# Kernel optimization log

Measured on AMD Instinct MI355X. Metric: run time of the kernel, lower is better.

The kernel has to match this reference:

```python
import jax, jax.numpy as jnp
import numpy as np

T, B, N, D, O = 128, 8, 512, 256, 1


def _xavier(key, shape):
    # matches nn.init.xavier_normal_ (gain=1): std = sqrt(2/(fan_in+fan_out))
    std = np.sqrt(2.0 / (shape[0] + shape[1])).astype(np.float32)
    return jax.random.normal(key, shape, jnp.float32) * std


def setup_inputs() -> dict:
    key = jax.random.key(0)
    ks = jax.random.split(key, 7)
    return {
        "x": jax.random.normal(ks[0], (T, B, D), jnp.float32),
        "w_mult": _xavier(ks[1], (N, D)),
        "b_mult": _xavier(ks[2], (N, 1))[:, 0],   # stored (N,1) in torch; used as bias vector
        "w_add": _xavier(ks[3], (N, N)),
        "b_add": _xavier(ks[4], (N, 1))[:, 0],
        "w_final": _xavier(ks[5], (O, N)),
        "b_final": _xavier(ks[6], (O, 1))[:, 0],
        "lmbda_mult": jnp.float32(1.0),
        "lmbda_add": jnp.float32(1.0),
        "eta_mult": jnp.float32(-0.5),
        "eta_add": jnp.float32(-0.5),
        "Store": 0,
        "Batch": 0,
    }


def reference(x, w_mult, b_mult, w_add, b_add, w_final, b_final,
              lmbda_mult, lmbda_add, eta_mult, eta_add, Store, Batch):
    # Store=False / Batch=False branch of HebbFF, vmapped over B sequences
    # and scanned over T timesteps. Fast-weight state: A_mult [B,N,D], A_add [B,N,N].
    Bt = x.shape[1]
    Nh, Dd = w_mult.shape
    lam_m = jax.nn.sigmoid(lmbda_mult)
    lam_a = jax.nn.sigmoid(lmbda_add)

    def step(carry, x_t):
        A_m, A_a = carry                      # [B,N,D], [B,N,N]
        # h_mult = tanh((w_mult * A_mult) @ x + w_mult @ x + b_mult)
        h_m = jnp.tanh(jnp.einsum('bnd,bd->bn', w_mult * A_m, x_t)
                       + x_t @ w_mult.T + b_mult)          # [B,N]
        A_m = lam_m * A_m + eta_mult * jnp.einsum('bn,bd->bnd', h_m, x_t)
        # h_add = sigmoid((w_add + A_add) @ h_mult + b_add)
        h_a = jax.nn.sigmoid(jnp.einsum('bnm,bm->bn', A_a, h_m)
                             + h_m @ w_add.T + b_add)      # [B,N]
        A_a = lam_a * A_a + eta_add * jnp.einsum('bn,bm->bnm', h_a, h_m)
        y_t = jax.nn.sigmoid(h_a @ w_final.T + b_final)    # [B,O]
        return (A_m, A_a), y_t

    A_m0 = jnp.zeros((Bt, Nh, Dd), x.dtype)
    A_a0 = jnp.zeros((Bt, Nh, Nh), x.dtype)
    _, ys = jax.lax.scan(step, (A_m0, A_a0), x)            # ys: [T,B,O]
    return ys
```

## Files before the change

kernel.cpp:

```cpp
#include <hip/hip_runtime.h>
#include <cstdint>


#define T_ 128
#define B_ 8
#define N_ 512
#define D_ 256
#define NTHREADS 512
#define CH 16
#define NC (T_ / CH)
#define HOFF (T_ * B_ * N_)

typedef float v2f __attribute__((ext_vector_type(2)));

__device__ __forceinline__ v2f v2(float s) { v2f r; r.x = s; r.y = s; return r; }

__device__ __forceinline__ void load_lds16(const float* g, float* l) {
  __builtin_amdgcn_global_load_lds(
      (const __attribute__((address_space(1))) uint32_t*)(const void*)g,
      (__attribute__((address_space(3))) uint32_t*)(void*)l, 16, 0, 0);
}

__device__ __forceinline__ float dpp_wave_sum(float v) {
#define UPD(ctrl)                                                              \
  v += __int_as_float(                                                         \
      __builtin_amdgcn_update_dpp(0, __float_as_int(v), ctrl, 0xf, 0xf, true))
  UPD(0x111); UPD(0x112); UPD(0x114); UPD(0x118); UPD(0x142); UPD(0x143);
#undef UPD
  return __int_as_float(__builtin_amdgcn_readlane(__float_as_int(v), 63));
}
__device__ __forceinline__ float sigmoid_f(float z) {
  return __builtin_amdgcn_rcpf(1.f + __expf(-z));
}
__device__ __forceinline__ float tanh_f(float z) {
  return 1.f - 2.f * __builtin_amdgcn_rcpf(1.f + __expf(2.f * z));
}

__global__ void __launch_bounds__(NTHREADS, 2)
hebb_part1(const float* __restrict__ x, const float* __restrict__ w_mult,
           const float* __restrict__ b_mult, const float* __restrict__ p_lm,
           const float* __restrict__ p_em, float* __restrict__ ws) {
  const int g = blockIdx.x & 7, sub = blockIdx.x >> 3;
  const int wave = threadIdx.x >> 6, lane = threadIdx.x & 63;
  const int n0 = (sub * 8 + wave) * 2;

  __shared__ float xs[2][CH][D_];

  const float lam = sigmoid_f(p_lm[0]);
  const float eta = p_em[0];
  const v2f lam2 = v2(lam), klam2 = v2(1.f - lam);

  v2f wm[2][2], Bm[2][2];
  float bm[2];
#pragma unroll
  for (int r = 0; r < 2; ++r) {
    bm[r] = b_mult[n0 + r];
#pragma unroll
    for (int c = 0; c < 2; ++c) {
      wm[r][c] = *(const v2f*)&w_mult[(n0 + r) * D_ + c * 128 + 2 * lane];
      Bm[r][c] = v2(1.f);
    }
  }

  auto issue_stage = [&](int c) {
#pragma unroll
    for (int k = 0; k < 2; ++k) {
      const int row = k * 8 + wave;
      const int trow = c * CH + row;
      load_lds16(&x[(trow * B_ + g) * D_ + 4 * lane], &xs[c & 1][row][0]);
    }
  };

  issue_stage(0);
  __syncthreads();

  v2f xv[2][2];
  auto ldx = [&](int buf, int cb, int tl) {
    xv[buf][0] = *(const v2f*)&xs[cb][tl][2 * lane];
    xv[buf][1] = *(const v2f*)&xs[cb][tl][128 + 2 * lane];
  };

  for (int c = 0; c < NC; ++c) {
    if (c + 1 < NC) issue_stage(c + 1);
    const int cb = c & 1;
    ldx(0, cb, 0);
#pragma unroll
    for (int tl = 0; tl < CH; ++tl) {
      const int buf = tl & 1;
      if (tl + 1 < CH) ldx(buf ^ 1, cb, tl + 1);
      float hmv[2];
#pragma unroll
      for (int r = 0; r < 2; ++r) {
        v2f a = wm[r][0] * xv[buf][0] * Bm[r][0];
        a = __builtin_elementwise_fma(wm[r][1] * xv[buf][1], Bm[r][1], a);
        const float z = dpp_wave_sum(a.x + a.y) + bm[r];
        const float hm = tanh_f(z);
        hmv[r] = hm;
        const v2f c2 = v2(eta * hm);
#pragma unroll
        for (int cc = 0; cc < 2; ++cc) {
          v2f inner = __builtin_elementwise_fma(c2, xv[buf][cc], klam2);
          Bm[r][cc] = __builtin_elementwise_fma(lam2, Bm[r][cc], inner);
        }
      }
      if (lane == 0) {
        v2f hv2; hv2.x = hmv[0]; hv2.y = hmv[1];
        *(v2f*)(ws + ((c * CH + tl) * B_ + g) * N_ + n0) = hv2;
      }
    }
    __syncthreads();
  }
}

__global__ void __launch_bounds__(NTHREADS, 2)
hebb_part2(const float* __restrict__ w_add, const float* __restrict__ b_add,
           const float* __restrict__ w_final, const float* __restrict__ p_la,
           const float* __restrict__ p_ea, float* __restrict__ ws) {
  const int g = blockIdx.x & 7, sub = blockIdx.x >> 3;
  const int wave = threadIdx.x >> 6, lane = threadIdx.x & 63;
  const int n0 = (sub * 8 + wave) * 2;

  __shared__ float hs[2][CH][N_];

  const float lam = sigmoid_f(p_la[0]);
  const float eta = p_ea[0];
  const v2f lam2 = v2(lam);
  const float klam = 1.f - lam;

  v2f Sa[2][4], wb[2][4];
  float ba[2], wf[2];
#pragma unroll
  for (int r = 0; r < 2; ++r) {
    ba[r] = b_add[n0 + r];
    wf[r] = w_final[n0 + r];
#pragma unroll
    for (int c = 0; c < 4; ++c) {
      const v2f wa = *(const v2f*)&w_add[(n0 + r) * N_ + c * 128 + 2 * lane];
      Sa[r][c] = wa;
      wb[r][c] = wa * klam;
    }
  }

  const float* hsrc = ws;
  float* part = ws + HOFF;

  auto issue_stage = [&](int c) {
#pragma unroll
    for (int k = 0; k < 2; ++k) {
      const int row = k * 8 + wave;
      const int trow = c * CH + row;
#pragma unroll
      for (int j = 0; j < 2; ++j)
        load_lds16(&hsrc[(trow * B_ + g) * N_ + j * 256 + 4 * lane],
                   &hs[c & 1][row][j * 256]);
    }
  };

  issue_stage(0);
  __syncthreads();

  v2f hv[2][4];
  auto ldh = [&](int buf, int cb, int tl) {
#pragma unroll
    for (int cc = 0; cc < 4; ++cc)
      hv[buf][cc] = *(const v2f*)&hs[cb][tl][cc * 128 + 2 * lane];
  };

  for (int c = 0; c < NC; ++c) {
    if (c + 1 < NC) issue_stage(c + 1);
    const int cb = c & 1;
    ldh(0, cb, 0);
#pragma unroll
    for (int tl = 0; tl < CH; ++tl) {
      const int buf = tl & 1;
      if (tl + 1 < CH) ldh(buf ^ 1, cb, tl + 1);
      float py = 0.f;
#pragma unroll
      for (int r = 0; r < 2; ++r) {
        v2f a0 = Sa[r][0] * hv[buf][0];
        v2f a1 = Sa[r][1] * hv[buf][1];
        a0 = __builtin_elementwise_fma(Sa[r][2], hv[buf][2], a0);
        a1 = __builtin_elementwise_fma(Sa[r][3], hv[buf][3], a1);
        const v2f a = a0 + a1;
        const float z = dpp_wave_sum(a.x + a.y) + ba[r];
        const float ha = sigmoid_f(z);
        const v2f c2 = v2(eta * ha);
#pragma unroll
        for (int cc = 0; cc < 4; ++cc) {
          v2f inner = __builtin_elementwise_fma(c2, hv[buf][cc], wb[r][cc]);
          Sa[r][cc] = __builtin_elementwise_fma(lam2, Sa[r][cc], inner);
        }
        py = __builtin_fmaf(wf[r], ha, py);
      }
      if (lane == 0)
        part[((c * CH + tl) * B_ + g) * 256 + sub * 8 + wave] = py;
    }
    __syncthreads();
  }
}

__global__ void __launch_bounds__(NTHREADS)
hebb_final(const float* __restrict__ ws, const float* __restrict__ b_final,
           float* __restrict__ out) {
  const int wave = threadIdx.x >> 6, lane = threadIdx.x & 63;
  const int tb = blockIdx.x * 8 + wave;
  const float4 v = *(const float4*)(ws + HOFF + tb * 256 + lane * 4);
  const float s = dpp_wave_sum((v.x + v.y) + (v.z + v.w));
  if (lane == 0) out[tb] = sigmoid_f(s + b_final[0]);
}

extern "C" void kernel_launch(void* const* d_in, const int* in_sizes, int n_in,
                              void* d_out, int out_size, void* d_ws,
                              size_t ws_size, hipStream_t stream) {
  const float* x       = (const float*)d_in[0];
  const float* w_mult  = (const float*)d_in[1];
  const float* b_mult  = (const float*)d_in[2];
  const float* w_add   = (const float*)d_in[3];
  const float* b_add   = (const float*)d_in[4];
  const float* w_final = (const float*)d_in[5];
  const float* b_final = (const float*)d_in[6];
  const float* p_lm    = (const float*)d_in[7];
  const float* p_la    = (const float*)d_in[8];
  const float* p_em    = (const float*)d_in[9];
  const float* p_ea    = (const float*)d_in[10];
  float* out = (float*)d_out;
  float* ws  = (float*)d_ws;

  hipLaunchKernelGGL(hebb_part1, dim3(256), dim3(NTHREADS), 0, stream,
                     x, w_mult, b_mult, p_lm, p_em, ws);
  hipLaunchKernelGGL(hebb_part2, dim3(256), dim3(NTHREADS), 0, stream,
                     w_add, b_add, w_final, p_la, p_ea, ws);
  hipLaunchKernelGGL(hebb_final, dim3(128), dim3(NTHREADS), 0, stream,
                     ws, b_final, out);
}
```

Baseline: 76.65 us.

## Replace additive fast-weight recurrence with unrolled kernel-matrix formulation and blocked scan

The additive Hebbian recurrence is rewritten algebraically. The A_add state contribution becomes a sum over past steps, weighted by lambda powers times the h_mult Gram products. A mid kernel computes w_add·h_mult for all timesteps plus the decayed Gram matrix, then a small scan kernel resolves the sigmoid recurrence in 16-step blocks, and a final kernel applies w_final. This removes the per-step N×N state update but adds an extra launch, O(T²) Gram work and a serial scan with limited parallelism (64 blocks). The old path is kept as a fallback when the workspace is too small.

```diff
diff --git a/kernel.cpp b/kernel.cpp
--- a/kernel.cpp
+++ b/kernel.cpp
@@ -9,11 +9,18 @@
 #define NTHREADS 512
 #define CH 16
 #define NC (T_ / CH)
+
+#define HP_OFF 0
+#define Z0_OFF 524288
+#define WS_OFF 1048576
+#define WS_NEED ((size_t)(1048576 + 131072) * 4)
+
 #define HOFF (T_ * B_ * N_)
 
 typedef float v2f __attribute__((ext_vector_type(2)));
 
 __device__ __forceinline__ v2f v2(float s) { v2f r; r.x = s; r.y = s; return r; }
+__device__ __forceinline__ v2f mk2(float a, float b) { v2f r; r.x = a; r.y = b; return r; }
 
 __device__ __forceinline__ void load_lds16(const float* g, float* l) {
   __builtin_amdgcn_global_load_lds(
@@ -36,14 +43,14 @@
   return 1.f - 2.f * __builtin_amdgcn_rcpf(1.f + __expf(2.f * z));
 }
 
+
 __global__ void __launch_bounds__(NTHREADS, 2)
-hebb_part1(const float* __restrict__ x, const float* __restrict__ w_mult,
-           const float* __restrict__ b_mult, const float* __restrict__ p_lm,
-           const float* __restrict__ p_em, float* __restrict__ ws) {
+np_part1(const float* __restrict__ x, const float* __restrict__ w_mult,
+         const float* __restrict__ b_mult, const float* __restrict__ p_lm,
+         const float* __restrict__ p_em, float* __restrict__ ws) {
   const int g = blockIdx.x & 7, sub = blockIdx.x >> 3;
   const int wave = threadIdx.x >> 6, lane = threadIdx.x & 63;
   const int n0 = (sub * 8 + wave) * 2;
-
   __shared__ float xs[2][CH][D_];
 
   const float lam = sigmoid_f(p_lm[0]);
@@ -66,20 +73,21 @@
 #pragma unroll
     for (int k = 0; k < 2; ++k) {
       const int row = k * 8 + wave;
-      const int trow = c * CH + row;
-      load_lds16(&x[(trow * B_ + g) * D_ + 4 * lane], &xs[c & 1][row][0]);
-    }
-  };
-
+      load_lds16(&x[((c * CH + row) * B_ + g) * D_ + 4 * lane],
+                 &xs[c & 1][row][0]);
+    }
+  };
   issue_stage(0);
   __syncthreads();
 
+  float* hp = ws + HP_OFF;
   v2f xv[2][2];
   auto ldx = [&](int buf, int cb, int tl) {
     xv[buf][0] = *(const v2f*)&xs[cb][tl][2 * lane];
     xv[buf][1] = *(const v2f*)&xs[cb][tl][128 + 2 * lane];
   };
 
+  float ph0 = 0.f, ph1 = 0.f;
   for (int c = 0; c < NC; ++c) {
     if (c + 1 < NC) issue_stage(c + 1);
     const int cb = c & 1;
@@ -103,8 +111,252 @@
           Bm[r][cc] = __builtin_elementwise_fma(lam2, Bm[r][cc], inner);
         }
       }
+      if (tl & 1) {
+        if (lane == 0) {
+          const int t2 = (c * CH + tl) >> 1;
+          *(float4*)(hp + ((t2 * B_ + g) * N_ + n0) * 2) =
+              make_float4(ph0, hmv[0], ph1, hmv[1]);
+        }
+      } else {
+        ph0 = hmv[0];
+        ph1 = hmv[1];
+      }
+    }
+    __syncthreads();
+  }
+}
+
+__global__ void __launch_bounds__(NTHREADS, 2)
+np_mid(const float* __restrict__ w_add, const float* __restrict__ b_add,
+       const float* __restrict__ p_la, const float* __restrict__ p_ea,
+       float* __restrict__ ws) {
+  __shared__ float hl[8192];
+  const int tid = threadIdx.x;
+  const int wave = tid >> 6, lane = tid & 63;
+  const float* hp = ws + HP_OFF;
+  float* z0 = ws + Z0_OFF;
+  float* Wsc = ws + WS_OFF;
+  const float lam = sigmoid_f(p_la[0]);
+  const float eta = p_ea[0];
+
+  if (blockIdx.x < 128) {
+    const int tbc = blockIdx.x;
+    const float* src = hp + tbc * 4 * 1024;
+#pragma unroll
+    for (int i = 0; i < 2; ++i)
+      load_lds16(src + (wave * 2 + i) * 256 + lane * 4,
+                 hl + (wave * 2 + i) * 256);
+    __syncthreads();
+    const int n = tid;
+    v2f acc[4] = {v2(0.f), v2(0.f), v2(0.f), v2(0.f)};
+    const float* wrow = w_add + n * N_;
+    for (int m = 0; m < N_; m += 4) {
+      const float4 w4 = *(const float4*)&wrow[m];
+#pragma unroll
+      for (int p = 0; p < 4; ++p) {
+        const float4 ha = *(const float4*)&hl[p * 1024 + m * 2];
+        const float4 hb = *(const float4*)&hl[p * 1024 + m * 2 + 4];
+        acc[p] = __builtin_elementwise_fma(v2(w4.x), mk2(ha.x, ha.y), acc[p]);
+        acc[p] = __builtin_elementwise_fma(v2(w4.y), mk2(ha.z, ha.w), acc[p]);
+        acc[p] = __builtin_elementwise_fma(v2(w4.z), mk2(hb.x, hb.y), acc[p]);
+        acc[p] = __builtin_elementwise_fma(v2(w4.w), mk2(hb.z, hb.w), acc[p]);
+      }
+    }
+    const float bad = b_add[n];
+#pragma unroll
+    for (int p = 0; p < 4; ++p) {
+      const int tbp = tbc * 4 + p;
+      const int tbe = tbp + 8 * (tbp >> 3);
+      z0[tbe * N_ + n] = acc[p].x + bad;
+      z0[(tbe + 8) * N_ + n] = acc[p].y + bad;
+    }
+  } else {
+    const int gb = blockIdx.x - 128;
+    const int b = gb >> 3, tc = gb & 7;
+    {
+      const int q = wave;
+      const float* rsrc = hp + ((tc * 8 + q) * 8 + b) * 1024;
+#pragma unroll
+      for (int sgm = 0; sgm < 4; ++sgm)
+        load_lds16(rsrc + sgm * 256 + lane * 4, hl + q * 1024 + sgm * 256);
+    }
+    __syncthreads();
+    const int s = tid & 127, tq = tid >> 7;
+    const int tmax = tc * 16 + tq * 4 + 3;
+    v2f acc[2] = {v2(0.f), v2(0.f)};
+    if (s < tmax) {
+      const float* srow = hp + ((s >> 1) * 8 + b) * 1024 + (s & 1);
+#pragma unroll 4
+      for (int n = 0; n < N_; ++n) {
+        const float hs = srow[n * 2];
+        const float2 hA = *(const float2*)&hl[(tq * 2 + 0) * 1024 + n * 2];
+        const float2 hB = *(const float2*)&hl[(tq * 2 + 1) * 1024 + n * 2];
+        acc[0] = __builtin_elementwise_fma(v2(hs), mk2(hA.x, hA.y), acc[0]);
+        acc[1] = __builtin_elementwise_fma(v2(hs), mk2(hB.x, hB.y), acc[1]);
+      }
+    }
+    const float l2lam = __log2f(lam);
+#pragma unroll
+    for (int i = 0; i < 4; ++i) {
+      const int t = tc * 16 + tq * 4 + i;
+      const float gv = (i & 1) ? acc[i >> 1].y : acc[i >> 1].x;
+      float w = 0.f;
+      if (s < t) w = eta * exp2f((float)(t - 1 - s) * l2lam) * gv;
+      Wsc[(b * T_ + t) * T_ + s] = w;
+    }
+  }
+}
+
+__global__ void __launch_bounds__(NTHREADS, 1)
+np_scan(float* __restrict__ ws) {
+  __shared__ float ul[T_][64];
+  __shared__ float zx[16][64];
+  __shared__ float Wtile[16][16];
+  const int b = blockIdx.x >> 3, nc = blockIdx.x & 7;
+  const int wave = threadIdx.x >> 6, lane = threadIdx.x & 63;
+  float* z0 = ws + Z0_OFF;
+  const float* Wb = ws + WS_OFF + b * T_ * T_;
+
+  const int ta = 2 * wave, tb2 = 2 * wave + 1;
+  const int ncol = nc * 64 + lane;
+
+  float za = z0[(ta * B_ + b) * N_ + ncol];
+  float zb = z0[(tb2 * B_ + b) * N_ + ncol];
+
+  for (int j = 0; j < 8; ++j) {
+    const int t0 = j * 16;
+    const float* wga = Wb + (t0 + ta) * T_;
+    const float* wgb = Wb + (t0 + tb2) * T_;
+    float zna = 0.f, znb = 0.f;
+    if (j < 7) {
+      zna = z0[((t0 + 16 + ta) * B_ + b) * N_ + ncol];
+      znb = z0[((t0 + 16 + tb2) * B_ + b) * N_ + ncol];
+    }
+    if (lane < 4) {
+      *(float4*)&Wtile[ta][lane * 4] = *(const float4*)&wga[t0 + lane * 4];
+      *(float4*)&Wtile[tb2][lane * 4] = *(const float4*)&wgb[t0 + lane * 4];
+    }
+    float ha0 = 0.f, ha1 = 0.f, hb0 = 0.f, hb1 = 0.f;
+#pragma unroll 2
+    for (int s4 = 0; s4 < t0; s4 += 4) {
+      const float4 wa = *(const float4*)&wga[s4];
+      const float4 wb = *(const float4*)&wgb[s4];
+      const float u0 = ul[s4 + 0][lane], u1 = ul[s4 + 1][lane];
+      const float u2 = ul[s4 + 2][lane], u3 = ul[s4 + 3][lane];
+      ha0 = __builtin_fmaf(wa.x, u0, ha0);
+      ha1 = __builtin_fmaf(wa.y, u1, ha1);
+      ha0 = __builtin_fmaf(wa.z, u2, ha0);
+      ha1 = __builtin_fmaf(wa.w, u3, ha1);
+      hb0 = __builtin_fmaf(wb.x, u0, hb0);
+      hb1 = __builtin_fmaf(wb.y, u1, hb1);
+      hb0 = __builtin_fmaf(wb.z, u2, hb0);
+      hb1 = __builtin_fmaf(wb.w, u3, hb1);
+    }
+    zx[ta][lane] = za + (ha0 + ha1);
+    zx[tb2][lane] = zb + (hb0 + hb1);
+    __syncthreads();
+    if (wave == 0) {
+      float z[16], uv[16];
+#pragma unroll
+      for (int i = 0; i < 16; ++i) z[i] = zx[i][lane];
+#pragma unroll
+      for (int i = 0; i < 16; ++i) {
+        const float u = sigmoid_f(z[i]);
+        uv[i] = u;
+        z0[((t0 + i) * B_ + b) * N_ + ncol] = u;
+#pragma unroll
+        for (int tt = i + 1; tt < 16; ++tt)
+          z[tt] = __builtin_fmaf(u, Wtile[tt][i], z[tt]);
+      }
+#pragma unroll
+      for (int i = 0; i < 16; ++i) ul[t0 + i][lane] = uv[i];
+    }
+    __syncthreads();
+    za = zna;
+    zb = znb;
+  }
+}
+
+__global__ void __launch_bounds__(NTHREADS)
+np_final(const float* __restrict__ ws, const float* __restrict__ w_final,
+         const float* __restrict__ b_final, float* __restrict__ out) {
+  const int wave = threadIdx.x >> 6, lane = threadIdx.x & 63;
+  const int tb = blockIdx.x * 8 + wave;
+  const float* u = ws + Z0_OFF + tb * N_ + lane * 8;
+  const float4 a = *(const float4*)u, c = *(const float4*)(u + 4);
+  const float4 wa = *(const float4*)&w_final[lane * 8];
+  const float4 wc = *(const float4*)&w_final[lane * 8 + 4];
+  float d = a.x * wa.x + a.y * wa.y + a.z * wa.z + a.w * wa.w +
+            c.x * wc.x + c.y * wc.y + c.z * wc.z + c.w * wc.w;
+  d = dpp_wave_sum(d);
+  if (lane == 0) out[tb] = sigmoid_f(d + b_final[0]);
+}
+
+
+__global__ void __launch_bounds__(NTHREADS, 2)
+fb_part1(const float* __restrict__ x, const float* __restrict__ w_mult,
+         const float* __restrict__ b_mult, const float* __restrict__ p_lm,
+         const float* __restrict__ p_em, float* __restrict__ ws) {
+  const int g = blockIdx.x & 7, sub = blockIdx.x >> 3;
+  const int wave = threadIdx.x >> 6, lane = threadIdx.x & 63;
+  const int n0 = (sub * 8 + wave) * 2;
+  __shared__ float xs[2][CH][D_];
+  const float lam = sigmoid_f(p_lm[0]);
+  const float eta = p_em[0];
+  const v2f lam2 = v2(lam), klam2 = v2(1.f - lam);
+  v2f wm[2][2], Bm[2][2];
+  float bm[2];
+#pragma unroll
+  for (int r = 0; r < 2; ++r) {
+    bm[r] = b_mult[n0 + r];
+#pragma unroll
+    for (int c = 0; c < 2; ++c) {
+      wm[r][c] = *(const v2f*)&w_mult[(n0 + r) * D_ + c * 128 + 2 * lane];
+      Bm[r][c] = v2(1.f);
+    }
+  }
+  auto issue_stage = [&](int c) {
+#pragma unroll
+    for (int k = 0; k < 2; ++k) {
+      const int row = k * 8 + wave;
+      load_lds16(&x[((c * CH + row) * B_ + g) * D_ + 4 * lane],
+                 &xs[c & 1][row][0]);
+    }
+  };
+  issue_stage(0);
+  __syncthreads();
+  v2f xv[2][2];
+  auto ldx = [&](int buf, int cb, int tl) {
+    xv[buf][0] = *(const v2f*)&xs[cb][tl][2 * lane];
+    xv[buf][1] = *(const v2f*)&xs[cb][tl][128 + 2 * lane];
+  };
+  for (int c = 0; c < NC; ++c) {
+    if (c + 1 < NC) issue_stage(c + 1);
+    const int cb = c & 1;
+    ldx(0, cb, 0);
+#pragma unroll
+    for (int tl = 0; tl < CH; ++tl) {
+      const int buf = tl & 1;
+      if (tl + 1 < CH) ldx(buf ^ 1, cb, tl + 1);
+      float hmv[2];
+#pragma unroll
+      for (int r = 0; r < 2; ++r) {
+        v2f a = wm[r][0] * xv[buf][0] * Bm[r][0];
+        a = __builtin_elementwise_fma(wm[r][1] * xv[buf][1], Bm[r][1], a);
+        const float z = dpp_wave_sum(a.x + a.y) + bm[r];
+        const float hm = tanh_f(z);
+        hmv[r] = hm;
+        const v2f c2 = v2(eta * hm);
+#pragma unroll
+        for (int cc = 0; cc < 2; ++cc) {
+          v2f inner = __builtin_elementwise_fma(c2, xv[buf][cc], klam2);
+          Bm[r][cc] = __builtin_elementwise_fma(lam2, Bm[r][cc], inner);
+        }
+      }
       if (lane == 0) {
-        v2f hv2; hv2.x = hmv[0]; hv2.y = hmv[1];
+        v2f hv2;
+        hv2.x = hmv[0];
+        hv2.y = hmv[1];
         *(v2f*)(ws + ((c * CH + tl) * B_ + g) * N_ + n0) = hv2;
       }
     }
@@ -113,20 +365,17 @@
 }
 
 __global__ void __launch_bounds__(NTHREADS, 2)
-hebb_part2(const float* __restrict__ w_add, const float* __restrict__ b_add,
-           const float* __restrict__ w_final, const float* __restrict__ p_la,
-           const float* __restrict__ p_ea, float* __restrict__ ws) {
+fb_part2(const float* __restrict__ w_add, const float* __restrict__ b_add,
+         const float* __restrict__ w_final, const float* __restrict__ p_la,
+         const float* __restrict__ p_ea, float* __restrict__ ws) {
   const int g = blockIdx.x & 7, sub = blockIdx.x >> 3;
   const int wave = threadIdx.x >> 6, lane = threadIdx.x & 63;
   const int n0 = (sub * 8 + wave) * 2;
-
   __shared__ float hs[2][CH][N_];
-
   const float lam = sigmoid_f(p_la[0]);
   const float eta = p_ea[0];
   const v2f lam2 = v2(lam);
   const float klam = 1.f - lam;
-
   v2f Sa[2][4], wb[2][4];
   float ba[2], wf[2];
 #pragma unroll
@@ -140,32 +389,26 @@
       wb[r][c] = wa * klam;
     }
   }
-
   const float* hsrc = ws;
   float* part = ws + HOFF;
-
   auto issue_stage = [&](int c) {
 #pragma unroll
     for (int k = 0; k < 2; ++k) {
       const int row = k * 8 + wave;
-      const int trow = c * CH + row;
-#pragma unroll
-      for (int j = 0; j < 2; ++j)
-        load_lds16(&hsrc[(trow * B_ + g) * N_ + j * 256 + 4 * lane],
-                   &hs[c & 1][row][j * 256]);
-    }
-  };
-
+#pragma unroll
+      for (int jj = 0; jj < 2; ++jj)
+        load_lds16(&hsrc[((c * CH + row) * B_ + g) * N_ + jj * 256 + 4 * lane],
+                   &hs[c & 1][row][jj * 256]);
+    }
+  };
   issue_stage(0);
   __syncthreads();
-
   v2f hv[2][4];
   auto ldh = [&](int buf, int cb, int tl) {
 #pragma unroll
     for (int cc = 0; cc < 4; ++cc)
       hv[buf][cc] = *(const v2f*)&hs[cb][tl][cc * 128 + 2 * lane];
   };
-
   for (int c = 0; c < NC; ++c) {
     if (c + 1 < NC) issue_stage(c + 1);
     const int cb = c & 1;
@@ -200,14 +443,15 @@
 }
 
 __global__ void __launch_bounds__(NTHREADS)
-hebb_final(const float* __restrict__ ws, const float* __restrict__ b_final,
-           float* __restrict__ out) {
+fb_final(const float* __restrict__ ws, const float* __restrict__ b_final,
+         float* __restrict__ out) {
   const int wave = threadIdx.x >> 6, lane = threadIdx.x & 63;
   const int tb = blockIdx.x * 8 + wave;
   const float4 v = *(const float4*)(ws + HOFF + tb * 256 + lane * 4);
   const float s = dpp_wave_sum((v.x + v.y) + (v.z + v.w));
   if (lane == 0) out[tb] = sigmoid_f(s + b_final[0]);
 }
+
 
 extern "C" void kernel_launch(void* const* d_in, const int* in_sizes, int n_in,
                               void* d_out, int out_size, void* d_ws,
@@ -226,10 +470,20 @@
   float* out = (float*)d_out;
   float* ws  = (float*)d_ws;
 
-  hipLaunchKernelGGL(hebb_part1, dim3(256), dim3(NTHREADS), 0, stream,
-                     x, w_mult, b_mult, p_lm, p_em, ws);
-  hipLaunchKernelGGL(hebb_part2, dim3(256), dim3(NTHREADS), 0, stream,
-                     w_add, b_add, w_final, p_la, p_ea, ws);
-  hipLaunchKernelGGL(hebb_final, dim3(128), dim3(NTHREADS), 0, stream,
-                     ws, b_final, out);
-}
+  if (ws_size >= WS_NEED) {
+    hipLaunchKernelGGL(np_part1, dim3(256), dim3(NTHREADS), 0, stream,
+                       x, w_mult, b_mult, p_lm, p_em, ws);
+    hipLaunchKernelGGL(np_mid, dim3(192), dim3(NTHREADS), 0, stream,
+                       w_add, b_add, p_la, p_ea, ws);
+    hipLaunchKernelGGL(np_scan, dim3(64), dim3(NTHREADS), 0, stream, ws);
+    hipLaunchKernelGGL(np_final, dim3(128), dim3(NTHREADS), 0, stream,
+                       ws, w_final, b_final, out);
+  } else {
+    hipLaunchKernelGGL(fb_part1, dim3(256), dim3(NTHREADS), 0, stream,
+                       x, w_mult, b_mult, p_lm, p_em, ws);
+    hipLaunchKernelGGL(fb_part2, dim3(256), dim3(NTHREADS), 0, stream,
+                       w_add, b_add, w_final, p_la, p_ea, ws);
+    hipLaunchKernelGGL(fb_final, dim3(128), dim3(NTHREADS), 0, stream,
+                       ws, b_final, out);
+  }
+}
```

Result: slower. 175.4 us (+128.9%).
